# Kernel optimization log

Hardware: AMD Instinct MI355X
Metric: run time of the kernel (lower is better)

## Reference

```python
import jax, jax.numpy as jnp
import numpy as np
import math

HIDDEN = 2048
N_HEADS = 16
HEAD_DIM = HIDDEN // N_HEADS
BASE = 10000.0


def setup_inputs() -> dict:
    key = jax.random.key(0)
    ks = jax.random.split(key, 8)
    s = 1.0 / math.sqrt(HIDDEN)
    inp = {
        "hidden_states": jax.random.normal(ks[0], (2, 2048, HIDDEN), dtype=jnp.float32),
        "Wq": jax.random.normal(ks[1], (HIDDEN, HIDDEN), dtype=jnp.float32) * s,
        "bq": jax.random.normal(ks[2], (HIDDEN,), dtype=jnp.float32) * s,
        "Wk": jax.random.normal(ks[3], (HIDDEN, HIDDEN), dtype=jnp.float32) * s,
        "bk": jax.random.normal(ks[4], (HIDDEN,), dtype=jnp.float32) * s,
        "Wv": jax.random.normal(ks[5], (HIDDEN, HIDDEN), dtype=jnp.float32) * s,
        "bv": jax.random.normal(ks[6], (HIDDEN,), dtype=jnp.float32) * s,
        "Wo": jax.random.normal(ks[7], (HIDDEN, HIDDEN), dtype=jnp.float32) * s,
    }
    return inp


def _rotate_half(x):
    x1, x2 = x[..., : x.shape[-1] // 2], x[..., x.shape[-1] // 2 :]
    return jnp.concatenate((-x2, x1), axis=-1)


def _rope_cos_sin(seq_len, dtype):
    inv_freq = 1.0 / (BASE ** (jnp.arange(0, HEAD_DIM, 2, dtype=jnp.float32) / HEAD_DIM))
    t = jnp.arange(seq_len, dtype=jnp.float32)
    freqs = jnp.einsum("i,j->ij", t, inv_freq)  # [S, head_dim/2]
    emb = jnp.concatenate((freqs, freqs), axis=-1)  # [S, head_dim]
    return jnp.cos(emb).astype(dtype), jnp.sin(emb).astype(dtype)


def reference(hidden_states, Wq, bq, Wk, bk, Wv, bv, Wo):
    B, S, _ = hidden_states.shape
    q = hidden_states @ Wq + bq
    k = hidden_states @ Wk + bk
    v = hidden_states @ Wv + bv
    # [B, H, S, D]
    q = q.reshape(B, S, N_HEADS, HEAD_DIM).transpose(0, 2, 1, 3)
    k = k.reshape(B, S, N_HEADS, HEAD_DIM).transpose(0, 2, 1, 3)
    v = v.reshape(B, S, N_HEADS, HEAD_DIM).transpose(0, 2, 1, 3)
    cos, sin = _rope_cos_sin(S, q.dtype)  # [S, D]
    cos = cos[None, None]
    sin = sin[None, None]
    q = q * cos + _rotate_half(q) * sin
    k = k * cos + _rotate_half(k) * sin
    scale = 1.0 / math.sqrt(HEAD_DIM)
    scores = jnp.einsum("bhqd,bhkd->bhqk", q, k) * scale
    attn = jax.nn.softmax(scores, axis=-1)
    out = jnp.einsum("bhqk,bhkd->bhqd", attn, v)
    out = out.transpose(0, 2, 1, 3).reshape(B, S, HIDDEN)
    return out @ Wo
```

## Files before the change

kernel.cpp:

```cpp
#include <hip/hip_runtime.h>

#define HID 2048
#define SEQ 2048
#define HD 128
#define QKN 6144

typedef float f32x4 __attribute__((ext_vector_type(4)));
typedef short s16x8 __attribute__((ext_vector_type(8)));
typedef __bf16 bf16x8 __attribute__((ext_vector_type(8)));

static __device__ __forceinline__ unsigned short f2bf(float x) {
    unsigned u = __float_as_uint(x);
    u = u + 0x7FFFu + ((u >> 16) & 1u);
    return (unsigned short)(u >> 16);
}
static __device__ __forceinline__ float bf2f(unsigned short h) {
    return __uint_as_float(((unsigned)h) << 16);
}
static __device__ __forceinline__ bf16x8 as_bf(s16x8 v) {
    union { s16x8 s; bf16x8 b; } u; u.s = v; return u.b;
}
static __device__ __forceinline__ bf16x8 ld_bf8(const unsigned short* p) {
    return as_bf(*(const s16x8*)p);
}
static __device__ __forceinline__ void gload_lds16(const void* g, void* l) {
    __builtin_amdgcn_global_load_lds(
        (const __attribute__((address_space(1))) void*)g,
        (__attribute__((address_space(3))) void*)l,
        16, 0, 0);
}

__global__ __launch_bounds__(256) void fill_f32(
    float* __restrict__ out, float v, int n)
{
    int i = blockIdx.x * 256 + threadIdx.x;
    if (i < n) out[i] = v;
}

__global__ __launch_bounds__(256) void convert_f32_bf16(
    const float* __restrict__ in, unsigned short* __restrict__ out)
{
    long i = ((long)blockIdx.x * 256 + threadIdx.x) * 8;
    f32x4 a = *(const f32x4*)&in[i];
    f32x4 b = *(const f32x4*)&in[i + 4];
    s16x8 o;
#pragma unroll
    for (int e = 0; e < 4; ++e) {
        o[e]     = (short)f2bf(a[e]);
        o[e + 4] = (short)f2bf(b[e]);
    }
    *(s16x8*)&out[i] = o;
}

__global__ __launch_bounds__(256) void transpose_w(
    const float* __restrict__ W, unsigned short* __restrict__ Wt)
{
    __shared__ float t[32][33];
    int k0 = blockIdx.x * 32, n0 = blockIdx.y * 32;
    int tx = threadIdx.x & 31, ty = threadIdx.x >> 5;
#pragma unroll
    for (int r = ty; r < 32; r += 8)
        t[r][tx] = W[(long)(k0 + r) * HID + n0 + tx];
    __syncthreads();
#pragma unroll
    for (int r = ty; r < 32; r += 8)
        Wt[(long)(n0 + r) * HID + k0 + tx] = f2bf(t[tx][r]);
}

template<int NF, bool F32OUT>
__global__ __launch_bounds__(512, 2) void gemm_8phase(
    const unsigned short* __restrict__ A,
    const unsigned short* __restrict__ Bt,
    const float* __restrict__ bq, const float* __restrict__ bk,
    const float* __restrict__ bv,
    unsigned short* __restrict__ Cb, float* __restrict__ Cf,
    int K, int ldc, int nbn, int sm, int sn, int hasBias)
{
    constexpr int BUFE = 16384 + NF * 4096;
    __shared__ unsigned short lds[2 * BUFE];
    const int tid = threadIdx.x;
    const int wid = tid >> 6, lane = tid & 63;
    const int l16 = lane & 15, l4 = lane >> 4;
    const int wm = wid >> 2, wn = wid & 3;

    const int bid = blockIdx.x;
    const int xcd = bid & 7, idx = bid >> 3;
    const int ncn = nbn / sn;
    const int cm = xcd / ncn, cn = xcd % ncn;
    const int lm = idx / sn,  ln = idx % sn;
    const long bm = (long)(cm * sm + lm) * 256;
    const long bn = (long)(cn * sn + ln) * (NF * 64);

    const int NT = K >> 6;
    const long strideB = (long)K * 2;
    const int srow = tid >> 3;
    const int scb  = ((tid & 7) * 16) ^ ((srow & 7) << 4);

    auto stageA = [&](int t, int c) {
        unsigned short* base = &lds[(t & 1) * BUFE];
        const int row = c * 64 + srow;
        const char* src = (const char*)A + (bm + row) * strideB + (long)t * 128 + scb;
        gload_lds16(src, base + (c * 64 + wid * 8) * 64);
    };
    auto stageB = [&](int t, int c) {
        unsigned short* base = &lds[(t & 1) * BUFE + 16384];
        const int row = c * 64 + srow;
        const char* src = (const char*)Bt + (bn + row) * strideB + (long)t * 128 + scb;
        gload_lds16(src, base + (c * 64 + wid * 8) * 64);
    };

    f32x4 acc[8][NF];
#pragma unroll
    for (int i = 0; i < 8; ++i)
#pragma unroll
        for (int j = 0; j < NF; ++j) acc[i][j] = f32x4{0.f, 0.f, 0.f, 0.f};

    auto compute = [&](const unsigned short* Ab, const unsigned short* Bb) {
#pragma unroll
        for (int kk = 0; kk < 2; ++kk) {
            bf16x8 bfr[NF];
#pragma unroll
            for (int j = 0; j < NF; ++j) {
                const int row = wn * (NF * 16) + j * 16 + l16;
                const char* rb = (const char*)Bb + row * 128;
                bfr[j] = as_bf(*(const s16x8*)(rb + ((kk * 64 + l4 * 16) ^ ((l16 & 7) << 4))));
            }
#pragma unroll
            for (int half = 0; half < 2; ++half) {
                bf16x8 af[4];
#pragma unroll
                for (int i = 0; i < 4; ++i) {
                    const int row = wm * 128 + (half * 4 + i) * 16 + l16;
                    const char* rb = (const char*)Ab + row * 128;
                    af[i] = as_bf(*(const s16x8*)(rb + ((kk * 64 + l4 * 16) ^ ((l16 & 7) << 4))));
                }
                __builtin_amdgcn_s_setprio(1);
#pragma unroll
                for (int i = 0; i < 4; ++i)
#pragma unroll
                    for (int j = 0; j < NF; ++j)
                        acc[half * 4 + i][j] = __builtin_amdgcn_mfma_f32_16x16x32_bf16(
                            af[i], bfr[j], acc[half * 4 + i][j], 0, 0, 0);
                __builtin_amdgcn_s_setprio(0);
            }
        }
    };

#pragma unroll
    for (int c = 0; c < 4; ++c) stageA(0, c);
#pragma unroll
    for (int c = 0; c < NF; ++c) stageB(0, c);

    for (int t = 0; t < NT - 1; ++t) {
        const unsigned short* Ab = &lds[(t & 1) * BUFE];
        const unsigned short* Bb = Ab + 16384;
#pragma unroll
        for (int c = 0; c < 4; ++c) stageA(t + 1, c);
#pragma unroll
        for (int c = 0; c < NF; ++c) stageB(t + 1, c);
        __builtin_amdgcn_sched_barrier(0);
        if constexpr (NF == 6)      asm volatile("s_waitcnt vmcnt(10)" ::: "memory");
        else if constexpr (NF == 3) asm volatile("s_waitcnt vmcnt(7)" ::: "memory");
        else                        asm volatile("s_waitcnt vmcnt(6)" ::: "memory");
        __builtin_amdgcn_s_barrier();
        __builtin_amdgcn_sched_barrier(0);
        compute(Ab, Bb);
        __builtin_amdgcn_s_barrier();
    }
    {
        const unsigned short* Ab = &lds[((NT - 1) & 1) * BUFE];
        const unsigned short* Bb = Ab + 16384;
        asm volatile("s_waitcnt vmcnt(0)" ::: "memory");
        __builtin_amdgcn_s_barrier();
        __builtin_amdgcn_sched_barrier(0);
        compute(Ab, Bb);
    }

    float bvv[NF];
#pragma unroll
    for (int nf = 0; nf < NF; ++nf) {
        const long n = bn + wn * (NF * 16) + nf * 16 + l16;
        bvv[nf] = 0.f;
        if (hasBias)
            bvv[nf] = (n < HID) ? bq[n] : ((n < 2 * HID) ? bk[n - HID] : bv[n - 2 * HID]);
    }
#pragma unroll
    for (int mf = 0; mf < 8; ++mf) {
#pragma unroll
        for (int r = 0; r < 4; ++r) {
            const long m = bm + wm * 128 + mf * 16 + l4 * 4 + r;
#pragma unroll
            for (int nf = 0; nf < NF; ++nf) {
                const long n = bn + wn * (NF * 16) + nf * 16 + l16;
                float v = acc[mf][nf][r] + bvv[nf];
                if (F32OUT) Cf[m * (long)ldc + n] = v;
                else        Cb[m * (long)ldc + n] = f2bf(v);
            }
        }
    }
}

__global__ __launch_bounds__(256) void rope_kernel(unsigned short* __restrict__ qkv)
{
    int t = blockIdx.x * 256 + threadIdx.x;
    int j8 = t & 7;
    int h  = (t >> 3) & 15;
    int qk = (t >> 7) & 1;
    int row = t >> 8;
    int s = row & (SEQ - 1);
    unsigned short* p = &qkv[(long)row * QKN + qk * HID + h * HD + j8 * 8];
    s16x8 lo = *(const s16x8*)p;
    s16x8 hi = *(const s16x8*)(p + 64);
    float qscale = qk ? 1.0f : 0.12751744581845f;
    s16x8 olo, ohi;
#pragma unroll
    for (int e = 0; e < 8; ++e) {
        int j = j8 * 8 + e;
        float inv = exp2f(-(float)j * 0.20762050593046f);
        float sn, cs;
        sincosf((float)s * inv, &sn, &cs);
        float x1 = bf2f((unsigned short)lo[e]);
        float x2 = bf2f((unsigned short)hi[e]);
        olo[e] = (short)f2bf((x1 * cs - x2 * sn) * qscale);
        ohi[e] = (short)f2bf((x2 * cs + x1 * sn) * qscale);
    }
    *(s16x8*)p = olo;
    *(s16x8*)(p + 64) = ohi;
}

__global__ __launch_bounds__(256) void v_transpose(
    const unsigned short* __restrict__ qkv, unsigned short* __restrict__ vt)
{
    __shared__ unsigned short t[32][33];
    int bh = blockIdx.z;
    int b = bh >> 4, h = bh & 15;
    int s0 = blockIdx.x * 32, d0 = blockIdx.y * 32;
    int tx = threadIdx.x & 31, ty = threadIdx.x >> 5;
#pragma unroll
    for (int r = ty; r < 32; r += 8)
        t[r][tx] = qkv[(long)(b * SEQ + s0 + r) * QKN + 2 * HID + h * HD + d0 + tx];
    __syncthreads();
#pragma unroll
    for (int r = ty; r < 32; r += 8)
        vt[((long)bh * HD + d0 + r) * SEQ + s0 + tx] = t[tx][r];
}

__global__ __launch_bounds__(512) void attn_kernel(
    const unsigned short* __restrict__ qkv,
    const unsigned short* __restrict__ vt,
    unsigned short* __restrict__ attnout)
{
    __shared__ unsigned short Ks[2][64 * 128];
    __shared__ unsigned short Vs[2][128 * 64];

    const int tid = threadIdx.x, wid = tid >> 6, lane = tid & 63;
    const int l16 = lane & 15, l4 = lane >> 4;
    const int bid = blockIdx.x;
    const int xcd = bid & 7, idx = bid >> 3;
    const int bh = xcd * 4 + (idx >> 4);
    const int qt = idx & 15;
    const int b = bh >> 4, h = bh & 15;
    const long rowbase = (long)b * SEQ;

    const unsigned short* Kg = &qkv[rowbase * QKN + HID + h * HD];
    const unsigned short* Vg = &vt[(long)bh * HD * SEQ];

    auto stage = [&](int buf, int kv0) {
#pragma unroll
        for (int i = 0; i < 2; ++i) {
            int c = wid * 2 + i;
            int kr = c * 4 + l4;
            int kcb = (l16 * 16) ^ ((kr & 7) << 4);
            gload_lds16((const char*)(Kg + (long)(kv0 + kr) * QKN) + kcb, &Ks[buf][c * 512]);
            int vr = c * 8 + (lane >> 3);
            int vcb = ((lane & 7) * 16) ^ ((vr & 7) << 4);
            gload_lds16((const char*)(Vg + (long)vr * SEQ + kv0) + vcb, &Vs[buf][c * 512]);
        }
    };

    bf16x8 qf[4];
    {
        const long qrow = rowbase + qt * 128 + wid * 16 + l16;
        const unsigned short* qp = &qkv[qrow * QKN + h * HD];
#pragma unroll
        for (int kc = 0; kc < 4; ++kc) qf[kc] = ld_bf8(qp + kc * 32 + l4 * 8);
    }

    f32x4 o[8];
#pragma unroll
    for (int nb = 0; nb < 8; ++nb) o[nb] = f32x4{0.f, 0.f, 0.f, 0.f};
    float mrun = -3.0e38f, lrun = 0.f;

    const int srcA = ((l4 & 1) * 2) * 16 + l16;
    const int srcB = srcA + 16;
    const bool sel = (l4 >> 1) != 0;

    stage(0, 0);
    __syncthreads();

    for (int t = 0; t < SEQ / 64; ++t) {
        const int cur = t & 1;
        if (t < SEQ / 64 - 1) stage(cur ^ 1, (t + 1) * 64);
        __builtin_amdgcn_sched_barrier(0);

        const unsigned short* Kc = &Ks[cur][0];
        const unsigned short* Vc = &Vs[cur][0];

        f32x4 sc[4];
#pragma unroll
        for (int nf = 0; nf < 4; ++nf) sc[nf] = f32x4{0.f, 0.f, 0.f, 0.f};
#pragma unroll
        for (int kc = 0; kc < 4; ++kc) {
#pragma unroll
            for (int nf = 0; nf < 4; ++nf) {
                int row = nf * 16 + l16;
                int cb = (kc * 64 + l4 * 16) ^ ((row & 7) << 4);
                bf16x8 kf = as_bf(*(const s16x8*)((const char*)Kc + row * 256 + cb));
                sc[nf] = __builtin_amdgcn_mfma_f32_16x16x32_bf16(kf, qf[kc], sc[nf], 0, 0, 0);
            }
        }

        float m0 = fmaxf(fmaxf(sc[0][0], sc[0][1]), sc[0][2]);
        float m1 = fmaxf(fmaxf(sc[0][3], sc[1][0]), sc[1][1]);
        float m2 = fmaxf(fmaxf(sc[1][2], sc[1][3]), sc[2][0]);
        float m3 = fmaxf(fmaxf(sc[2][1], sc[2][2]), sc[2][3]);
        float m4 = fmaxf(fmaxf(sc[3][0], sc[3][1]), sc[3][2]);
        float tmax = fmaxf(fmaxf(m0, m1), m2);
        tmax = fmaxf(fmaxf(m3, m4), tmax);
        tmax = fmaxf(tmax, sc[3][3]);
        tmax = fmaxf(tmax, __shfl_xor(tmax, 16, 64));
        tmax = fmaxf(tmax, __shfl_xor(tmax, 32, 64));

        if (!__all(tmax - mrun <= 8.0f)) {
            float mn = fmaxf(mrun, tmax);
            float sc_ = exp2f(mrun - mn);
            mrun = mn;
            lrun *= sc_;
            float s_[4];
#pragma unroll
            for (int r = 0; r < 4; ++r) s_[r] = __shfl(sc_, l4 * 4 + r, 64);
#pragma unroll
            for (int nb = 0; nb < 8; ++nb)
#pragma unroll
                for (int r = 0; r < 4; ++r) o[nb][r] *= s_[r];
        }

        unsigned pk[4][2];
        float sum = 0.f;
#pragma unroll
        for (int nf = 0; nf < 4; ++nf) {
            float p0 = exp2f(sc[nf][0] - mrun);
            float p1 = exp2f(sc[nf][1] - mrun);
            float p2 = exp2f(sc[nf][2] - mrun);
            float p3 = exp2f(sc[nf][3] - mrun);
            sum += (p0 + p1) + (p2 + p3);
            union { __bf16 b[2]; unsigned u; } w0, w1;
            w0.b[0] = (__bf16)p0; w0.b[1] = (__bf16)p1;
            w1.b[0] = (__bf16)p2; w1.b[1] = (__bf16)p3;
            pk[nf][0] = w0.u; pk[nf][1] = w1.u;
        }
        sum += __shfl_xor(sum, 16, 64);
        sum += __shfl_xor(sum, 32, 64);
        lrun += sum;

        union { unsigned u[4]; bf16x8 v; } pa0, pa1;
#pragma unroll
        for (int w = 0; w < 2; ++w) {
            unsigned a0 = __shfl(pk[0][w], srcA, 64);
            unsigned a1 = __shfl(pk[1][w], srcA, 64);
            unsigned b0 = __shfl(pk[0][w], srcB, 64);
            unsigned b1 = __shfl(pk[1][w], srcB, 64);
            pa0.u[w]     = sel ? a1 : a0;
            pa0.u[2 + w] = sel ? b1 : b0;
            unsigned c0 = __shfl(pk[2][w], srcA, 64);
            unsigned c1 = __shfl(pk[3][w], srcA, 64);
            unsigned d0 = __shfl(pk[2][w], srcB, 64);
            unsigned d1 = __shfl(pk[3][w], srcB, 64);
            pa1.u[w]     = sel ? c1 : c0;
            pa1.u[2 + w] = sel ? d1 : d0;
        }

#pragma unroll
        for (int kc = 0; kc < 2; ++kc) {
            bf16x8 pav = kc ? pa1.v : pa0.v;
#pragma unroll
            for (int nb = 0; nb < 8; ++nb) {
                int vrow = nb * 16 + l16;
                int vcb = (kc * 64 + l4 * 16) ^ ((vrow & 7) << 4);
                bf16x8 vb = as_bf(*(const s16x8*)((const char*)Vc + vrow * 128 + vcb));
                o[nb] = __builtin_amdgcn_mfma_f32_16x16x32_bf16(pav, vb, o[nb], 0, 0, 0);
            }
        }
        __syncthreads();
    }

    float linv = 1.f / lrun;
    float li[4];
#pragma unroll
    for (int r = 0; r < 4; ++r) li[r] = __shfl(linv, l4 * 4 + r, 64);
#pragma unroll
    for (int r = 0; r < 4; ++r) {
        long m = rowbase + qt * 128 + wid * 16 + l4 * 4 + r;
#pragma unroll
        for (int nb = 0; nb < 8; ++nb)
            attnout[m * HID + h * HD + nb * 16 + l16] = f2bf(o[nb][r] * li[r]);
    }
}

extern "C" void kernel_launch(void* const* d_in, const int* in_sizes, int n_in,
                              void* d_out, int out_size, void* d_ws, size_t ws_size,
                              hipStream_t stream)
{
    const float* hs = (const float*)d_in[0];
    const float* Wq = (const float*)d_in[1];
    const float* bq = (const float*)d_in[2];
    const float* Wk = (const float*)d_in[3];
    const float* bk = (const float*)d_in[4];
    const float* Wv = (const float*)d_in[5];
    const float* bv = (const float*)d_in[6];
    const float* Wo = (const float*)d_in[7];
    float* out = (float*)d_out;

    bool shapes_ok =
        (n_in == 8) && (out_size == 8388608) &&
        in_sizes[0] == 8388608 && in_sizes[1] == 4194304 && in_sizes[2] == 2048 &&
        in_sizes[3] == 4194304 && in_sizes[4] == 2048 && in_sizes[5] == 4194304 &&
        in_sizes[6] == 2048 && in_sizes[7] == 4194304;
    if (!shapes_ok || ws_size < 117440512ull) {
        fill_f32<<<32768, 256, 0, stream>>>(out, shapes_ok ? 1000.f : 0.f, out_size);
        return;
    }

    char* ws = (char*)d_ws;
    unsigned short* hsB     = (unsigned short*)(ws);
    unsigned short* qkvB    = (unsigned short*)(ws + 16777216);
    unsigned short* wqkvT   = (unsigned short*)(ws + 67108864);
    unsigned short* vtB     = (unsigned short*)(ws + 92274688);
    unsigned short* woT     = (unsigned short*)(ws + 109051904);
    unsigned short* attnout = hsB;

    convert_f32_bf16<<<4096, 256, 0, stream>>>(hs, hsB);
    dim3 tg(64, 64);
    transpose_w<<<tg, 256, 0, stream>>>(Wq, wqkvT);
    transpose_w<<<tg, 256, 0, stream>>>(Wk, wqkvT + 2048 * 2048);
    transpose_w<<<tg, 256, 0, stream>>>(Wv, wqkvT + 2 * 2048 * 2048);
    transpose_w<<<tg, 256, 0, stream>>>(Wo, woT);

    gemm_8phase<6, false><<<dim3(256), 512, 0, stream>>>(
        hsB, wqkvT, bq, bk, bv, qkvB, nullptr, 2048, QKN, 16, 8, 4, 1);
    rope_kernel<<<4096, 256, 0, stream>>>(qkvB);
    v_transpose<<<dim3(64, 4, 32), 256, 0, stream>>>(qkvB, vtB);
    attn_kernel<<<dim3(512), 512, 0, stream>>>(qkvB, vtB, attnout);
    gemm_8phase<2, true><<<dim3(256), 512, 0, stream>>>(
        attnout, woT, nullptr, nullptr, nullptr, nullptr, out, 2048, HID, 16, 4, 8, 0);
}
```

Before: 300.8 us.

## Fuse RoPE and query scaling into the QKV GEMM epilogue

Removes the separate rope_kernel pass over the Q/K portion of the QKV buffer. The GEMM epilogue now stages each 64-row chunk of accumulators through LDS in fp32 and applies the rotary embedding and query scale there, then writes bf16 output with head-aligned columns. This saves a full read and write of Q and K plus one kernel launch. In exchange the epilogue gains extra barriers, LDS traffic and per-row sincos work, and the global stores are now laid out per 64-column half instead of per fragment.

Result: no change. 297.7 us (-1.0%).

```diff
diff --git a/kernel.cpp b/kernel.cpp
--- a/kernel.cpp
+++ b/kernel.cpp
@@ -67,7 +67,7 @@
         Wt[(long)(n0 + r) * HID + k0 + tx] = f2bf(t[tx][r]);
 }
 
-template<int NF, bool F32OUT>
+template<int NF, bool F32OUT, bool ROPE>
 __global__ __launch_bounds__(512, 2) void gemm_8phase(
     const unsigned short* __restrict__ A,
     const unsigned short* __restrict__ Bt,
@@ -184,48 +184,67 @@
         if (hasBias)
             bvv[nf] = (n < HID) ? bq[n] : ((n < 2 * HID) ? bk[n - HID] : bv[n - 2 * HID]);
     }
-#pragma unroll
-    for (int mf = 0; mf < 8; ++mf) {
-#pragma unroll
-        for (int r = 0; r < 4; ++r) {
-            const long m = bm + wm * 128 + mf * 16 + l4 * 4 + r;
-#pragma unroll
-            for (int nf = 0; nf < NF; ++nf) {
-                const long n = bn + wn * (NF * 16) + nf * 16 + l16;
-                float v = acc[mf][nf][r] + bvv[nf];
-                if (F32OUT) Cf[m * (long)ldc + n] = v;
-                else        Cb[m * (long)ldc + n] = f2bf(v);
-            }
-        }
-    }
-}
-
-__global__ __launch_bounds__(256) void rope_kernel(unsigned short* __restrict__ qkv)
-{
-    int t = blockIdx.x * 256 + threadIdx.x;
-    int j8 = t & 7;
-    int h  = (t >> 3) & 15;
-    int qk = (t >> 7) & 1;
-    int row = t >> 8;
-    int s = row & (SEQ - 1);
-    unsigned short* p = &qkv[(long)row * QKN + qk * HID + h * HD + j8 * 8];
-    s16x8 lo = *(const s16x8*)p;
-    s16x8 hi = *(const s16x8*)(p + 64);
-    float qscale = qk ? 1.0f : 0.12751744581845f;
-    s16x8 olo, ohi;
-#pragma unroll
-    for (int e = 0; e < 8; ++e) {
-        int j = j8 * 8 + e;
-        float inv = exp2f(-(float)j * 0.20762050593046f);
-        float sn, cs;
-        sincosf((float)s * inv, &sn, &cs);
-        float x1 = bf2f((unsigned short)lo[e]);
-        float x2 = bf2f((unsigned short)hi[e]);
-        olo[e] = (short)f2bf((x1 * cs - x2 * sn) * qscale);
-        ohi[e] = (short)f2bf((x2 * cs + x1 * sn) * qscale);
-    }
-    *(s16x8*)p = olo;
-    *(s16x8*)(p + 64) = ohi;
+
+    if constexpr (ROPE) {
+        constexpr int NH = NF / 2;
+        float* fl = (float*)lds;
+        const int jr = tid & 63;
+        const int rquo = tid >> 6;
+        const float inv = exp2f(-(float)jr * 0.20762050593046f);
+#pragma unroll
+        for (int c = 0; c < 4; ++c) {
+            __builtin_amdgcn_s_barrier();
+            if (wm == (c >> 1)) {
+                const int mf0 = (c & 1) * 4;
+#pragma unroll
+                for (int mfi = 0; mfi < 4; ++mfi)
+#pragma unroll
+                    for (int r = 0; r < 4; ++r) {
+                        const int rl = mfi * 16 + l4 * 4 + r;
+#pragma unroll
+                        for (int nf = 0; nf < NF; ++nf)
+                            fl[rl * 385 + wn * (NF * 16) + nf * 16 + l16] =
+                                acc[mf0 + mfi][nf][r] + bvv[nf];
+                    }
+            }
+            __builtin_amdgcn_s_barrier();
+#pragma unroll
+            for (int rr = 0; rr < 8; ++rr) {
+                const int rl = rr * 8 + rquo;
+                const long m = bm + (c >> 1) * 128 + (c & 1) * 64 + rl;
+                const int s = (int)(m & (SEQ - 1));
+                float sn, cs;
+                sincosf((float)s * inv, &sn, &cs);
+#pragma unroll
+                for (int hh = 0; hh < NH; ++hh) {
+                    const long n = bn + hh * 128 + jr;
+                    const bool ron = n < 2 * HID;
+                    const float qsv = (n < HID) ? 0.12751744581845f : 1.0f;
+                    const float se = ron ? sn : 0.f;
+                    const float ce = ron ? cs : 1.f;
+                    const float x1 = fl[rl * 385 + hh * 128 + jr];
+                    const float x2 = fl[rl * 385 + hh * 128 + jr + 64];
+                    Cb[m * (long)ldc + n]      = f2bf((x1 * ce - x2 * se) * qsv);
+                    Cb[m * (long)ldc + n + 64] = f2bf((x2 * ce + x1 * se) * qsv);
+                }
+            }
+        }
+    } else {
+#pragma unroll
+        for (int mf = 0; mf < 8; ++mf) {
+#pragma unroll
+            for (int r = 0; r < 4; ++r) {
+                const long m = bm + wm * 128 + mf * 16 + l4 * 4 + r;
+#pragma unroll
+                for (int nf = 0; nf < NF; ++nf) {
+                    const long n = bn + wn * (NF * 16) + nf * 16 + l16;
+                    float v = acc[mf][nf][r] + bvv[nf];
+                    if (F32OUT) Cf[m * (long)ldc + n] = v;
+                    else        Cb[m * (long)ldc + n] = f2bf(v);
+                }
+            }
+        }
+    }
 }
 
 __global__ __launch_bounds__(256) void v_transpose(
@@ -446,11 +465,10 @@
     transpose_w<<<tg, 256, 0, stream>>>(Wv, wqkvT + 2 * 2048 * 2048);
     transpose_w<<<tg, 256, 0, stream>>>(Wo, woT);
 
-    gemm_8phase<6, false><<<dim3(256), 512, 0, stream>>>(
+    gemm_8phase<6, false, true><<<dim3(256), 512, 0, stream>>>(
         hsB, wqkvT, bq, bk, bv, qkvB, nullptr, 2048, QKN, 16, 8, 4, 1);
-    rope_kernel<<<4096, 256, 0, stream>>>(qkvB);
     v_transpose<<<dim3(64, 4, 32), 256, 0, stream>>>(qkvB, vtB);
     attn_kernel<<<dim3(512), 512, 0, stream>>>(qkvB, vtB, attnout);
-    gemm_8phase<2, true><<<dim3(256), 512, 0, stream>>>(
+    gemm_8phase<2, true, false><<<dim3(256), 512, 0, stream>>>(
         attnout, woT, nullptr, nullptr, nullptr, nullptr, out, 2048, HID, 16, 4, 8, 0);
 }
```
